# Kernel tuning notes

Hardware: AMD Instinct MI355X
Metric: run time of the kernel (lower is better)

## Reference

```python
import jax, jax.numpy as jnp
import numpy as np

# Fixed graph/model dims (see shape_source)
C = 16      # cardinality
SUB = 64    # representation_size // cardinality
R = 1024    # representation_size
E = 1024    # node_encoding_size
S = 1024    # processed spatial feature size
G = 256     # global (FPN) channels
NH = 64     # number of human nodes
N = 256     # total number of nodes (humans first)
P = NH * N  # number of (human, node) pairs
EPS = 1e-5


def _layernorm(x, g, b):
    mu = jnp.mean(x, axis=-1, keepdims=True)
    var = jnp.var(x, axis=-1, keepdims=True)
    return (x - mu) * jax.lax.rsqrt(var + EPS) * g + b


def _pair_head(app, spat, W1, b1, W2, b2, W3, b3):
    # app: [P_or_1, A], spat: [P, S] -> [P, R]  (sum over cardinality; NO outer relu)
    a1 = jnp.einsum('pi,cis->cps', app, W1) + b1[:, None, :]   # [C,P_or_1,SUB]
    a2 = jnp.einsum('pj,cjs->cps', spat, W2) + b2[:, None, :]  # [C,P,SUB]
    h = jax.nn.relu(a1 * a2)                                   # broadcast over P
    return jnp.einsum('cps,csr->pr', h, W3) + jnp.sum(b3, axis=0)


def reference(node_encodings, spatial_raw, global_feat,
              sp_W1, sp_b1, sp_W2, sp_b2, sp_W3, sp_b3,
              ah_W1, ah_b1, ah_W2, ah_b2, ah_W3, ah_b3,
              o2s_W1, o2s_b1, o2s_W2, o2s_b2, o2s_W3, o2s_b3,
              s2o_W1, s2o_b1, s2o_W2, s2o_b2, s2o_W3, s2o_b3,
              ahg_W1, ahg_b1, ahg_W2, ahg_b2, ahg_W3, ahg_b3,
              adj_W, adj_b, lnh_g, lnh_b, lno_g, lno_b):
    # spatial head MLP: 36 -> 128 -> 256 -> 1024 with ReLU
    sp = jax.nn.relu(spatial_raw @ sp_W1 + sp_b1)
    sp = jax.nn.relu(sp @ sp_W2 + sp_b2)
    sp = jax.nn.relu(sp @ sp_W3 + sp_b3)            # [P, S]
    sp3 = sp.reshape(NH, N, S)                      # [NH, N, S]

    x_idx = jnp.repeat(jnp.arange(NH), N)           # [P]
    y_idx = jnp.tile(jnp.arange(N), NH)             # [P]

    h_enc = node_encodings[:NH]                     # humans are permuted to the top
    o_enc = node_encodings

    for _ in range(1):  # num_iter
        app_pairs = jnp.concatenate([h_enc[x_idx], o_enc[y_idx]], axis=1)  # [P, 2E]
        weights = jax.nn.relu(_pair_head(app_pairs, sp, ah_W1, ah_b1, ah_W2, ah_b2, ah_W3, ah_b3))
        adj = (weights @ adj_W + adj_b).reshape(NH, N)

        # obj_to_sub (node_type='object'): appearance = all node encodings
        a1 = jnp.einsum('ni,cis->cns', o_enc, o2s_W1) + o2s_b1[:, None, :]          # [C,N,SUB]
        a2 = jnp.einsum('hnj,cjs->chns', sp3, o2s_W2) + o2s_b2[:, None, None, :]    # [C,NH,N,SUB]
        m = jnp.einsum('chns,csr->hnr', jax.nn.relu(a1[:, None] * a2), o2s_W3) + jnp.sum(o2s_b3, axis=0)
        msg_h = jax.nn.relu(jnp.sum(jax.nn.softmax(adj, axis=1)[..., None] * m, axis=1))  # [NH,R]
        h_enc = _layernorm(h_enc + msg_h, lnh_g, lnh_b)

        # sub_to_obj (node_type='human'): appearance = human encodings
        a1 = jnp.einsum('hi,cis->chs', h_enc, s2o_W1) + s2o_b1[:, None, :]          # [C,NH,SUB]
        a2 = jnp.einsum('hnj,cjs->cnhs', sp3, s2o_W2) + s2o_b2[:, None, None, :]    # [C,N,NH,SUB]
        m = jnp.einsum('cnhs,csr->nhr', jax.nn.relu(a1[:, None] * a2), s2o_W3) + jnp.sum(s2o_b3, axis=0)
        msg_o = jax.nn.relu(jnp.sum(jax.nn.softmax(adj.T, axis=1)[..., None] * m, axis=1))  # [N,R]
        o_enc = _layernorm(o_enc + msg_o, lno_g, lno_b)

    app_final = jnp.concatenate([h_enc[x_idx], o_enc[y_idx]], axis=1)               # [P, 2E]
    f_local = jax.nn.relu(_pair_head(app_final, sp, ah_W1, ah_b1, ah_W2, ah_b2, ah_W3, ah_b3))
    f_glob = jax.nn.relu(_pair_head(global_feat, sp, ahg_W1, ahg_b1, ahg_W2, ahg_b2, ahg_W3, ahg_b3))
    return jnp.concatenate([f_local, f_glob], axis=1)  # [P, 2R]


def setup_inputs() -> dict:
    key = jax.random.key(0)
    ks = iter(jax.random.split(key, 64))
    def rn(shape, scale=0.05):
        return jax.random.normal(next(ks), shape, dtype=jnp.float32) * scale
    inp = {
        'node_encodings': jax.random.normal(next(ks), (N, E), dtype=jnp.float32),
        'spatial_raw': jax.random.normal(next(ks), (P, 36), dtype=jnp.float32),
        'global_feat': jax.random.normal(next(ks), (1, G), dtype=jnp.float32),
        'sp_W1': rn((36, 128)), 'sp_b1': jnp.zeros(128, jnp.float32),
        'sp_W2': rn((128, 256)), 'sp_b2': jnp.zeros(256, jnp.float32),
        'sp_W3': rn((256, S)), 'sp_b3': jnp.zeros(S, jnp.float32),
        'ah_W1': rn((C, 2 * E, SUB)), 'ah_b1': jnp.zeros((C, SUB), jnp.float32),
        'ah_W2': rn((C, S, SUB)), 'ah_b2': jnp.zeros((C, SUB), jnp.float32),
        'ah_W3': rn((C, SUB, R)), 'ah_b3': jnp.zeros((C, R), jnp.float32),
        'o2s_W1': rn((C, E, SUB)), 'o2s_b1': jnp.zeros((C, SUB), jnp.float32),
        'o2s_W2': rn((C, S, SUB)), 'o2s_b2': jnp.zeros((C, SUB), jnp.float32),
        'o2s_W3': rn((C, SUB, R)), 'o2s_b3': jnp.zeros((C, R), jnp.float32),
        's2o_W1': rn((C, E, SUB)), 's2o_b1': jnp.zeros((C, SUB), jnp.float32),
        's2o_W2': rn((C, S, SUB)), 's2o_b2': jnp.zeros((C, SUB), jnp.float32),
        's2o_W3': rn((C, SUB, R)), 's2o_b3': jnp.zeros((C, R), jnp.float32),
        'ahg_W1': rn((C, G, SUB)), 'ahg_b1': jnp.zeros((C, SUB), jnp.float32),
        'ahg_W2': rn((C, S, SUB)), 'ahg_b2': jnp.zeros((C, SUB), jnp.float32),
        'ahg_W3': rn((C, SUB, R)), 'ahg_b3': jnp.zeros((C, R), jnp.float32),
        'adj_W': rn((R, 1)), 'adj_b': jnp.zeros(1, jnp.float32),
        'lnh_g': jnp.ones(E, jnp.float32), 'lnh_b': jnp.zeros(E, jnp.float32),
        'lno_g': jnp.ones(E, jnp.float32), 'lno_b': jnp.zeros(E, jnp.float32),
    }
    return inp
```

## Files before the change

### kernel.cpp

```cpp
#include <hip/hip_runtime.h>
#include <hip/hip_bf16.h>
#include <stdint.h>
#include <stddef.h>

using bf16 = __hip_bfloat16;
typedef __bf16 bf16x8 __attribute__((ext_vector_type(8)));
typedef float f32x4 __attribute__((ext_vector_type(4)));

#define P_  16384

__device__ __forceinline__ void gload16(const void* g, void* l) {
    __builtin_amdgcn_global_load_lds((const __attribute__((address_space(1))) void*)g,
                                     (__attribute__((address_space(3))) void*)l, 16, 0, 0);
}

template<int MODE, bool RELU, bool BIAS>
__global__ __launch_bounds__(256, 3)
void gemm_bt(const bf16* __restrict__ A, const bf16* __restrict__ B,
             void* __restrict__ C, const float* __restrict__ bias,
             const float* __restrict__ aux1, const float* __restrict__ aux2,
             int M, int N, int K, int ldc, int kchunk)
{
    __shared__ __align__(16) bf16 As[128 * 32];
    __shared__ __align__(16) bf16 Bs[128 * 32];

    const int tid  = threadIdx.x;
    const int wave = tid >> 6;
    const int lane = tid & 63;
    const int tileM = blockIdx.x * 128;
    const int tileN = blockIdx.y * 128;
    const int wr = (wave >> 1) << 6;
    const int wc = (wave & 1) << 6;

    f32x4 acc[4][4] = {};

    int arow[2], brow[2], ako[2];
    #pragma unroll
    for (int j = 0; j < 2; ++j) {
        int c  = wave * 128 + j * 64 + lane;
        int r  = c >> 2;
        ako[j] = (c & 3) << 3;
        int gr = tileM + r; if (gr > M - 1) gr = M - 1;
        arow[j] = gr;
        int gn = tileN + r; if (gn > N - 1) gn = N - 1;
        brow[j] = gn;
    }
    const int m0   = wr + (lane & 15);
    const int n0   = wc + (lane & 15);
    const int koff = (lane >> 4) << 3;

    int kbeg = 0, kend = K;
    if constexpr (MODE == 2) { kbeg = blockIdx.z * kchunk; kend = kbeg + kchunk; }

    for (int k0 = kbeg; k0 < kend; k0 += 32) {
        #pragma unroll
        for (int j = 0; j < 2; ++j) {
            int c = wave * 128 + j * 64 + lane;
            gload16(A + (size_t)arow[j] * K + k0 + ako[j], (void*)(As + c * 8));
            gload16(B + (size_t)brow[j] * K + k0 + ako[j], (void*)(Bs + c * 8));
        }
        __syncthreads();
        bf16x8 af[4], bfv[4];
        #pragma unroll
        for (int i = 0; i < 4; ++i) {
            af[i]  = *(const bf16x8*)(As + (m0 + i * 16) * 32 + koff);
            bfv[i] = *(const bf16x8*)(Bs + (n0 + i * 16) * 32 + koff);
        }
        #pragma unroll
        for (int i = 0; i < 4; ++i)
            #pragma unroll
            for (int j = 0; j < 4; ++j)
                acc[i][j] = __builtin_amdgcn_mfma_f32_16x16x32_bf16(af[i], bfv[j], acc[i][j], 0, 0, 0);
        __syncthreads();
    }

    const int rbase = tileM + wr + ((lane >> 4) << 2);
    const int cbase = tileN + wc + (lane & 15);

    if constexpr (MODE == 0 || MODE == 1) {
        #pragma unroll
        for (int i = 0; i < 4; ++i)
            #pragma unroll
            for (int j = 0; j < 4; ++j)
                #pragma unroll
                for (int r = 0; r < 4; ++r) {
                    int grow = rbase + i * 16 + r;
                    if (grow >= M) continue;
                    int gcol = cbase + j * 16;
                    float v = acc[i][j][r];
                    if (BIAS) v += bias[gcol];
                    if (RELU) v = fmaxf(v, 0.f);
                    if (MODE == 1) ((bf16*)C)[(size_t)grow * ldc + gcol] = __float2bfloat16(v);
                    else           ((float*)C)[(size_t)grow * ldc + gcol] = v;
                }
    } else if constexpr (MODE == 2) {
        #pragma unroll
        for (int i = 0; i < 4; ++i)
            #pragma unroll
            for (int j = 0; j < 4; ++j)
                #pragma unroll
                for (int r = 0; r < 4; ++r) {
                    int grow = rbase + i * 16 + r;
                    if (grow >= M) continue;
                    atomicAdd((float*)C + (size_t)grow * ldc + cbase + j * 16, acc[i][j][r]);
                }
    } else if constexpr (MODE >= 3 && MODE <= 5) {
        #pragma unroll
        for (int i = 0; i < 4; ++i)
            #pragma unroll
            for (int j = 0; j < 4; ++j)
                #pragma unroll
                for (int r = 0; r < 4; ++r) {
                    int p    = rbase + i * 16 + r;
                    int gcol = cbase + j * 16;
                    float a2v = acc[i][j][r] + bias[gcol];
                    float a1v;
                    if (MODE == 3) a1v = aux1[((size_t)(p & 255) << 10) + gcol] + aux2[gcol];
                    if (MODE == 4) a1v = aux1[((size_t)(p >> 8)  << 10) + gcol] + aux2[gcol];
                    if (MODE == 5) a1v = aux1[gcol];
                    float h = fmaxf(a1v * a2v, 0.f);
                    size_t orow = (MODE == 4) ? (size_t)((p & 255) * 64 + (p >> 8)) : (size_t)p;
                    ((bf16*)C)[orow * 1024 + gcol] = __float2bfloat16(h);
                }
    } else if constexpr (MODE == 6) {
        #pragma unroll
        for (int i = 0; i < 4; ++i)
            #pragma unroll
            for (int r = 0; r < 4; ++r) {
                float s = 0.f;
                #pragma unroll
                for (int j = 0; j < 4; ++j) {
                    int gcol = cbase + j * 16;
                    s += fmaxf(acc[i][j][r] + bias[gcol], 0.f) * aux1[gcol];
                }
                s += __shfl_xor(s, 1); s += __shfl_xor(s, 2);
                s += __shfl_xor(s, 4); s += __shfl_xor(s, 8);
                if ((lane & 15) == 0)
                    atomicAdd((float*)C + rbase + i * 16 + r, s);
            }
    } else {
        float s[4] = {0.f, 0.f, 0.f, 0.f};
        #pragma unroll
        for (int i = 0; i < 4; ++i)
            #pragma unroll
            for (int r = 0; r < 4; ++r) {
                float wv = aux1[rbase + i * 16 + r];
                #pragma unroll
                for (int j = 0; j < 4; ++j) s[j] += wv * acc[i][j][r];
            }
        #pragma unroll
        for (int j = 0; j < 4; ++j) {
            s[j] += __shfl_xor(s[j], 16);
            s[j] += __shfl_xor(s[j], 32);
        }
        if (lane < 16) {
            int outrow = (tileM + wr) >> (MODE == 7 ? 8 : 6);
            #pragma unroll
            for (int j = 0; j < 4; ++j)
                atomicAdd((float*)C + (size_t)outrow * 1024 + cbase + j * 16, s[j]);
        }
    }
}

__global__ void transp(const float* __restrict__ src, bf16* __restrict__ dst,
                       int rows, int cols, size_t sstride, size_t dstride)
{
    const float* s = src + blockIdx.z * sstride;
    bf16*        d = dst + blockIdx.z * dstride;
    __shared__ float tile[32][33];
    int c0 = blockIdx.x * 32, r0 = blockIdx.y * 32;
    int x = threadIdx.x, y = threadIdx.y;
    for (int yy = y; yy < 32; yy += 8) {
        int r = r0 + yy, c = c0 + x;
        tile[yy][x] = (r < rows && c < cols) ? s[(size_t)r * cols + c] : 0.f;
    }
    __syncthreads();
    for (int yy = y; yy < 32; yy += 8) {
        int c = c0 + yy, r = r0 + x;
        if (c < cols && r < rows) d[(size_t)c * rows + r] = __float2bfloat16(tile[x][yy]);
    }
}

__global__ void conv_spw1(const float* __restrict__ src, bf16* __restrict__ dst) {
    int i = blockIdx.x * 256 + threadIdx.x;
    if (i >= 128 * 64) return;
    int k = i & 63, n = i >> 6;
    dst[i] = __float2bfloat16(k < 36 ? src[k * 128 + n] : 0.f);
}

__global__ void pad_spatial(const float* __restrict__ src, bf16* __restrict__ dst) {
    int i = blockIdx.x * 256 + threadIdx.x;
    int k = i & 63, p = i >> 6;
    dst[i] = __float2bfloat16(k < 36 ? src[p * 36 + k] : 0.f);
}

__global__ void cast_f2b(const float* __restrict__ src, bf16* __restrict__ dst, int n) {
    int i = blockIdx.x * 256 + threadIdx.x;
    if (i < n) dst[i] = __float2bfloat16(src[i]);
}

__global__ void sumb3_k(const float* __restrict__ b3, float* __restrict__ out) {
    int r = blockIdx.x * 256 + threadIdx.x;
    float s = 0.f;
    #pragma unroll
    for (int c = 0; c < 16; ++c) s += b3[c * 1024 + r];
    out[r] = s;
}

__global__ void hbuild(const float* __restrict__ Ah, const float* __restrict__ Ao,
                       const float* __restrict__ b1, const bf16* __restrict__ a2,
                       bf16* __restrict__ H)
{
    size_t base = ((size_t)blockIdx.x * 256 + threadIdx.x) * 8;
    int cs = (int)(base & 1023);
    int p  = (int)(base >> 10);
    const float* ph = Ah + ((size_t)(p >> 8) << 10) + cs;
    const float* po = Ao + ((size_t)(p & 255) << 10) + cs;
    bf16x8 av = *(const bf16x8*)(a2 + base);
    bf16x8 o;
    #pragma unroll
    for (int j = 0; j < 8; ++j) {
        float a1 = ph[j] + po[j] + b1[cs + j];
        o[j] = (__bf16)fmaxf(a1 * (float)av[j], 0.f);
    }
    *(bf16x8*)(H + base) = o;
}

__global__ void softmax_h(const float* __restrict__ adj, float* __restrict__ sh) {
    int h = blockIdx.x, n = threadIdx.x;
    __shared__ float red[256];
    float v = adj[h * 256 + n];
    red[n] = v; __syncthreads();
    for (int s = 128; s > 0; s >>= 1) { if (n < s) red[n] = fmaxf(red[n], red[n + s]); __syncthreads(); }
    float m = red[0]; __syncthreads();
    float e = expf(v - m);
    red[n] = e; __syncthreads();
    for (int s = 128; s > 0; s >>= 1) { if (n < s) red[n] += red[n + s]; __syncthreads(); }
    sh[h * 256 + n] = e / red[0];
}

__global__ void softmax_o(const float* __restrict__ adj, float* __restrict__ so) {
    int n = blockIdx.x, h = threadIdx.x;
    float v = adj[h * 256 + n];
    float m = v;
    #pragma unroll
    for (int off = 32; off; off >>= 1) m = fmaxf(m, __shfl_xor(m, off));
    float e = expf(v - m);
    float s = e;
    #pragma unroll
    for (int off = 32; off; off >>= 1) s += __shfl_xor(s, off);
    so[n * 64 + h] = e / s;
}

__global__ void ln_k(const float* __restrict__ x, const float* __restrict__ msgraw,
                     const float* __restrict__ sb3,
                     const float* __restrict__ g, const float* __restrict__ bb,
                     bf16* __restrict__ out)
{
    int row = blockIdx.x, t = threadIdx.x;
    const float* xr = x + (size_t)row * 1024;
    const float* mr = msgraw + (size_t)row * 1024;
    float v[4]; float s = 0.f, ss = 0.f;
    #pragma unroll
    for (int j = 0; j < 4; ++j) {
        int i = t + j * 256;
        v[j] = xr[i] + fmaxf(mr[i] + sb3[i], 0.f);
        s += v[j]; ss += v[j] * v[j];
    }
    __shared__ float r1[256], r2[256];
    r1[t] = s; r2[t] = ss; __syncthreads();
    for (int k = 128; k > 0; k >>= 1) { if (t < k) { r1[t] += r1[t + k]; r2[t] += r2[t + k]; } __syncthreads(); }
    float mean = r1[0] * (1.f / 1024.f);
    float var  = r2[0] * (1.f / 1024.f) - mean * mean;
    float inv  = rsqrtf(var + 1e-5f);
    #pragma unroll
    for (int j = 0; j < 4; ++j) {
        int i = t + j * 256;
        out[(size_t)row * 1024 + i] = __float2bfloat16((v[j] - mean) * inv * g[i] + bb[i]);
    }
}

__global__ void a1g_k(const float* __restrict__ gf, const float* __restrict__ W1,
                      const float* __restrict__ b1, float* __restrict__ a1g)
{
    int cs = blockIdx.x * 256 + threadIdx.x;
    int c = cs >> 6, s = cs & 63;
    float acc = b1[cs];
    for (int g = 0; g < 256; ++g) acc += gf[g] * W1[((size_t)c * 256 + g) * 64 + s];
    a1g[cs] = acc;
}

extern "C" void kernel_launch(void* const* d_in, const int* in_sizes, int n_in,
                              void* d_out, int out_size, void* d_ws, size_t ws_size,
                              hipStream_t stream)
{
    const float* node_enc = (const float*)d_in[0];
    const float* spatial  = (const float*)d_in[1];
    const float* gfeat    = (const float*)d_in[2];
    const float* sp_W1 = (const float*)d_in[3];  const float* sp_b1 = (const float*)d_in[4];
    const float* sp_W2 = (const float*)d_in[5];  const float* sp_b2 = (const float*)d_in[6];
    const float* sp_W3 = (const float*)d_in[7];  const float* sp_b3 = (const float*)d_in[8];
    const float* ah_W1 = (const float*)d_in[9];  const float* ah_b1 = (const float*)d_in[10];
    const float* ah_W2 = (const float*)d_in[11]; const float* ah_b2 = (const float*)d_in[12];
    const float* ah_W3 = (const float*)d_in[13]; const float* ah_b3 = (const float*)d_in[14];
    const float* o2s_W1 = (const float*)d_in[15]; const float* o2s_b1 = (const float*)d_in[16];
    const float* o2s_W2 = (const float*)d_in[17]; const float* o2s_b2 = (const float*)d_in[18];
    const float* o2s_W3 = (const float*)d_in[19]; const float* o2s_b3 = (const float*)d_in[20];
    const float* s2o_W1 = (const float*)d_in[21]; const float* s2o_b1 = (const float*)d_in[22];
    const float* s2o_W2 = (const float*)d_in[23]; const float* s2o_b2 = (const float*)d_in[24];
    const float* s2o_W3 = (const float*)d_in[25]; const float* s2o_b3 = (const float*)d_in[26];
    const float* ahg_W1 = (const float*)d_in[27]; const float* ahg_b1 = (const float*)d_in[28];
    const float* ahg_W2 = (const float*)d_in[29]; const float* ahg_b2 = (const float*)d_in[30];
    const float* ahg_W3 = (const float*)d_in[31]; const float* ahg_b3 = (const float*)d_in[32];
    const float* adj_W = (const float*)d_in[33];
    const float* lnh_g = (const float*)d_in[35]; const float* lnh_b = (const float*)d_in[36];
    const float* lno_g = (const float*)d_in[37]; const float* lno_b = (const float*)d_in[38];

    char* w = (char*)d_ws;
    auto alloc = [&](size_t bytes) { char* p = w; w += (bytes + 255) & ~(size_t)255; return p; };
    bf16*  sp      = (bf16*)alloc((size_t)P_ * 1024 * 2);
    bf16*  a2_ah   = (bf16*)alloc((size_t)P_ * 1024 * 2);
    bf16*  Hbuf    = (bf16*)alloc((size_t)P_ * 1024 * 2);
    bf16*  spat_pad= (bf16*)alloc((size_t)P_ * 64 * 2);
    bf16*  spL1    = (bf16*)alloc((size_t)P_ * 128 * 2);
    bf16*  spL2    = (bf16*)alloc((size_t)P_ * 256 * 2);
    bf16*  enc_bf  = (bf16*)alloc(256 * 1024 * 2);
    bf16*  henc_bf = (bf16*)alloc(64 * 1024 * 2);
    bf16*  oenc_bf = (bf16*)alloc(256 * 1024 * 2);
    bf16*  spW1t   = (bf16*)alloc(128 * 64 * 2);
    bf16*  spW2t   = (bf16*)alloc(256 * 128 * 2);
    bf16*  spW3t   = (bf16*)alloc(1024 * 256 * 2);
    bf16*  ahW1tT  = (bf16*)alloc(1024 * 1024 * 2);
    bf16*  ahW1tB  = (bf16*)alloc(1024 * 1024 * 2);
    bf16*  ahW2t   = (bf16*)alloc(1024 * 1024 * 2);
    bf16*  ahW3t   = (bf16*)alloc(1024 * 1024 * 2);
    bf16*  o2sW1t  = (bf16*)alloc(1024 * 1024 * 2);
    bf16*  o2sW2t  = (bf16*)alloc(1024 * 1024 * 2);
    bf16*  o2sW3t  = (bf16*)alloc(1024 * 1024 * 2);
    bf16*  s2oW1t  = (bf16*)alloc(1024 * 1024 * 2);
    bf16*  s2oW2t  = (bf16*)alloc(1024 * 1024 * 2);
    bf16*  s2oW3t  = (bf16*)alloc(1024 * 1024 * 2);
    bf16*  ahgW2t  = (bf16*)alloc(1024 * 1024 * 2);
    bf16*  ahgW3t  = (bf16*)alloc(1024 * 1024 * 2);
    float* Ah    = (float*)alloc(64 * 1024 * 4);
    float* Ao    = (float*)alloc(256 * 1024 * 4);
    float* a1o2s = (float*)alloc(256 * 1024 * 4);
    float* a1s2o = (float*)alloc(64 * 1024 * 4);
    float* a1g   = (float*)alloc(1024 * 4);
    float* adjv  = (float*)alloc(P_ * 4);
    float* sh    = (float*)alloc(P_ * 4);
    float* so    = (float*)alloc(P_ * 4);
    float* msgh  = (float*)alloc(64 * 1024 * 4);
    float* msgo  = (float*)alloc(256 * 1024 * 4);
    float* sb3_ah  = (float*)alloc(4096);
    float* sb3_o2s = (float*)alloc(4096);
    float* sb3_s2o = (float*)alloc(4096);
    float* sb3_ahg = (float*)alloc(4096);

    hipMemsetAsync(Ah,   0, (64 + 256 + 256 + 64) * 1024 * 4, stream);
    hipMemsetAsync(adjv, 0, P_ * 4, stream);
    hipMemsetAsync(msgh, 0, 64 * 1024 * 4, stream);
    hipMemsetAsync(msgo, 0, 256 * 1024 * 4, stream);

    dim3 tb(32, 8);
    conv_spw1<<<32, 256, 0, stream>>>(sp_W1, spW1t);
    transp<<<dim3(8, 4, 1),  tb, 0, stream>>>(sp_W2, spW2t, 128, 256, 0, 0);
    transp<<<dim3(32, 8, 1), tb, 0, stream>>>(sp_W3, spW3t, 256, 1024, 0, 0);
    transp<<<dim3(2, 32, 16), tb, 0, stream>>>(ah_W1,                     ahW1tT, 1024, 64, (size_t)2048 * 64, (size_t)64 * 1024);
    transp<<<dim3(2, 32, 16), tb, 0, stream>>>(ah_W1 + (size_t)1024 * 64, ahW1tB, 1024, 64, (size_t)2048 * 64, (size_t)64 * 1024);
    transp<<<dim3(2, 32, 16), tb, 0, stream>>>(ah_W2,  ahW2t,  1024, 64, 65536, 65536);
    transp<<<dim3(2, 32, 16), tb, 0, stream>>>(o2s_W1, o2sW1t, 1024, 64, 65536, 65536);
    transp<<<dim3(2, 32, 16), tb, 0, stream>>>(o2s_W2, o2sW2t, 1024, 64, 65536, 65536);
    transp<<<dim3(2, 32, 16), tb, 0, stream>>>(s2o_W1, s2oW1t, 1024, 64, 65536, 65536);
    transp<<<dim3(2, 32, 16), tb, 0, stream>>>(s2o_W2, s2oW2t, 1024, 64, 65536, 65536);
    transp<<<dim3(2, 32, 16), tb, 0, stream>>>(ahg_W2, ahgW2t, 1024, 64, 65536, 65536);
    transp<<<dim3(32, 32, 1), tb, 0, stream>>>(ah_W3,  ahW3t,  1024, 1024, 0, 0);
    transp<<<dim3(32, 32, 1), tb, 0, stream>>>(o2s_W3, o2sW3t, 1024, 1024, 0, 0);
    transp<<<dim3(32, 32, 1), tb, 0, stream>>>(s2o_W3, s2oW3t, 1024, 1024, 0, 0);
    transp<<<dim3(32, 32, 1), tb, 0, stream>>>(ahg_W3, ahgW3t, 1024, 1024, 0, 0);
    pad_spatial<<<4096, 256, 0, stream>>>(spatial, spat_pad);
    cast_f2b<<<1024, 256, 0, stream>>>(node_enc, enc_bf, 256 * 1024);
    sumb3_k<<<4, 256, 0, stream>>>(ah_b3,  sb3_ah);
    sumb3_k<<<4, 256, 0, stream>>>(o2s_b3, sb3_o2s);
    sumb3_k<<<4, 256, 0, stream>>>(s2o_b3, sb3_s2o);
    sumb3_k<<<4, 256, 0, stream>>>(ahg_b3, sb3_ahg);
    a1g_k<<<4, 256, 0, stream>>>(gfeat, ahg_W1, ahg_b1, a1g);

    #define G128(M, N) dim3(((M) + 127) / 128, (N) / 128), dim3(256)
    #define GSPL(M)    dim3(((M) + 127) / 128, 8, 8), dim3(256)

    gemm_bt<1, true, true><<<G128(P_, 128),  0, stream>>>(spat_pad, spW1t, spL1, sp_b1, nullptr, nullptr, P_, 128, 64, 128, 0);
    gemm_bt<1, true, true><<<G128(P_, 256),  0, stream>>>(spL1,     spW2t, spL2, sp_b2, nullptr, nullptr, P_, 256, 128, 256, 0);
    gemm_bt<1, true, true><<<G128(P_, 1024), 0, stream>>>(spL2,     spW3t, sp,   sp_b3, nullptr, nullptr, P_, 1024, 256, 1024, 0);

    gemm_bt<1, false, true><<<G128(P_, 1024), 0, stream>>>(sp, ahW2t, a2_ah, ah_b2, nullptr, nullptr, P_, 1024, 1024, 1024, 0);

    gemm_bt<2, false, false><<<GSPL(64),  0, stream>>>(enc_bf, ahW1tT, Ah, nullptr, nullptr, nullptr, 64,  1024, 1024, 1024, 128);
    gemm_bt<2, false, false><<<GSPL(256), 0, stream>>>(enc_bf, ahW1tB, Ao, nullptr, nullptr, nullptr, 256, 1024, 1024, 1024, 128);
    hbuild<<<8192, 256, 0, stream>>>(Ah, Ao, ah_b1, a2_ah, Hbuf);
    gemm_bt<6, false, false><<<G128(P_, 1024), 0, stream>>>(Hbuf, ahW3t, adjv, sb3_ah, adj_W, nullptr, P_, 1024, 1024, 1024, 0);
    softmax_h<<<64, 256, 0, stream>>>(adjv, sh);
    softmax_o<<<256, 64, 0, stream>>>(adjv, so);

    gemm_bt<2, false, false><<<GSPL(256), 0, stream>>>(enc_bf, o2sW1t, a1o2s, nullptr, nullptr, nullptr, 256, 1024, 1024, 1024, 128);
    gemm_bt<3, false, false><<<G128(P_, 1024), 0, stream>>>(sp, o2sW2t, Hbuf, o2s_b2, a1o2s, o2s_b1, P_, 1024, 1024, 1024, 0);
    gemm_bt<7, false, false><<<G128(P_, 1024), 0, stream>>>(Hbuf, o2sW3t, msgh, nullptr, sh, nullptr, P_, 1024, 1024, 1024, 0);
    ln_k<<<64, 256, 0, stream>>>(node_enc, msgh, sb3_o2s, lnh_g, lnh_b, henc_bf);

    gemm_bt<2, false, false><<<GSPL(64), 0, stream>>>(henc_bf, s2oW1t, a1s2o, nullptr, nullptr, nullptr, 64, 1024, 1024, 1024, 128);
    gemm_bt<4, false, false><<<G128(P_, 1024), 0, stream>>>(sp, s2oW2t, Hbuf, s2o_b2, a1s2o, s2o_b1, P_, 1024, 1024, 1024, 0);
    gemm_bt<8, false, false><<<G128(P_, 1024), 0, stream>>>(Hbuf, s2oW3t, msgo, nullptr, so, nullptr, P_, 1024, 1024, 1024, 0);
    ln_k<<<256, 256, 0, stream>>>(node_enc, msgo, sb3_s2o, lno_g, lno_b, oenc_bf);

    hipMemsetAsync(Ah, 0, (64 + 256) * 1024 * 4, stream);
    gemm_bt<2, false, false><<<GSPL(64),  0, stream>>>(henc_bf, ahW1tT, Ah, nullptr, nullptr, nullptr, 64,  1024, 1024, 1024, 128);
    gemm_bt<2, false, false><<<GSPL(256), 0, stream>>>(oenc_bf, ahW1tB, Ao, nullptr, nullptr, nullptr, 256, 1024, 1024, 1024, 128);
    hbuild<<<8192, 256, 0, stream>>>(Ah, Ao, ah_b1, a2_ah, Hbuf);
    gemm_bt<0, true, true><<<G128(P_, 1024), 0, stream>>>(Hbuf, ahW3t, (float*)d_out, sb3_ah, nullptr, nullptr, P_, 1024, 1024, 2048, 0);

    gemm_bt<5, false, false><<<G128(P_, 1024), 0, stream>>>(sp, ahgW2t, Hbuf, ahg_b2, a1g, nullptr, P_, 1024, 1024, 1024, 0);
    gemm_bt<0, true, true><<<G128(P_, 1024), 0, stream>>>(Hbuf, ahgW3t, (float*)d_out + 1024, sb3_ahg, nullptr, nullptr, P_, 1024, 1024, 2048, 0);

    (void)in_sizes; (void)n_in; (void)out_size; (void)ws_size;
}
```

Measured before the change: 849.0 us.

## Batch W2 projections into one wide GEMM and merge W1 GEMMs and transposes

Concatenates the ah, o2s and ahg W2 weights so the spatial features are read once by a single N=3072 GEMM. Its epilogue writes a2_ah, the o2s hidden tensor and the ahg hidden tensor in one pass. W1 projections that share an input are merged into wider split-K GEMMs with smaller K chunks, and many small transpose, bias-sum and memset launches are batched into single kernels. This cuts repeated reads of the large sp activation and per-launch overhead. In exchange it allocates two extra P×1024 bf16 buffers and adds a branchy epilogue.

```diff
diff --git a/kernel.cpp b/kernel.cpp
--- a/kernel.cpp
+++ b/kernel.cpp
@@ -14,12 +14,20 @@
                                      (__attribute__((address_space(3))) void*)l, 16, 0, 0);
 }
 
+struct GArgs {
+    const bf16* A; const bf16* B; void* C;
+    const float* bias;
+    const float* aux1;
+    const float* aux2;
+    int M, N, K, ldc, kchunk, aux_ld;
+    void* C2; void* C3;
+    const float* b2a; const float* b2b; const float* b2c;
+    const float* b1o;  const float* a1gv;
+};
+
 template<int MODE, bool RELU, bool BIAS>
 __global__ __launch_bounds__(256, 3)
-void gemm_bt(const bf16* __restrict__ A, const bf16* __restrict__ B,
-             void* __restrict__ C, const float* __restrict__ bias,
-             const float* __restrict__ aux1, const float* __restrict__ aux2,
-             int M, int N, int K, int ldc, int kchunk)
+void gemm_bt(GArgs g)
 {
     __shared__ __align__(16) bf16 As[128 * 32];
     __shared__ __align__(16) bf16 Bs[128 * 32];
@@ -31,6 +39,7 @@
     const int tileN = blockIdx.y * 128;
     const int wr = (wave >> 1) << 6;
     const int wc = (wave & 1) << 6;
+    const int M = g.M, N = g.N, K = g.K;
 
     f32x4 acc[4][4] = {};
 
@@ -50,14 +59,14 @@
     const int koff = (lane >> 4) << 3;
 
     int kbeg = 0, kend = K;
-    if constexpr (MODE == 2) { kbeg = blockIdx.z * kchunk; kend = kbeg + kchunk; }
+    if constexpr (MODE == 2) { kbeg = blockIdx.z * g.kchunk; kend = kbeg + g.kchunk; }
 
     for (int k0 = kbeg; k0 < kend; k0 += 32) {
         #pragma unroll
         for (int j = 0; j < 2; ++j) {
             int c = wave * 128 + j * 64 + lane;
-            gload16(A + (size_t)arow[j] * K + k0 + ako[j], (void*)(As + c * 8));
-            gload16(B + (size_t)brow[j] * K + k0 + ako[j], (void*)(Bs + c * 8));
+            gload16(g.A + (size_t)arow[j] * K + k0 + ako[j], (void*)(As + c * 8));
+            gload16(g.B + (size_t)brow[j] * K + k0 + ako[j], (void*)(Bs + c * 8));
         }
         __syncthreads();
         bf16x8 af[4], bfv[4];
@@ -88,10 +97,10 @@
                     if (grow >= M) continue;
                     int gcol = cbase + j * 16;
                     float v = acc[i][j][r];
-                    if (BIAS) v += bias[gcol];
+                    if (BIAS) v += g.bias[gcol];
                     if (RELU) v = fmaxf(v, 0.f);
-                    if (MODE == 1) ((bf16*)C)[(size_t)grow * ldc + gcol] = __float2bfloat16(v);
-                    else           ((float*)C)[(size_t)grow * ldc + gcol] = v;
+                    if (MODE == 1) ((bf16*)g.C)[(size_t)grow * g.ldc + gcol] = __float2bfloat16(v);
+                    else           ((float*)g.C)[(size_t)grow * g.ldc + gcol] = v;
                 }
     } else if constexpr (MODE == 2) {
         #pragma unroll
@@ -102,9 +111,9 @@
                 for (int r = 0; r < 4; ++r) {
                     int grow = rbase + i * 16 + r;
                     if (grow >= M) continue;
-                    atomicAdd((float*)C + (size_t)grow * ldc + cbase + j * 16, acc[i][j][r]);
+                    atomicAdd((float*)g.C + (size_t)grow * g.ldc + cbase + j * 16, acc[i][j][r]);
                 }
-    } else if constexpr (MODE >= 3 && MODE <= 5) {
+    } else if constexpr (MODE == 4) {
         #pragma unroll
         for (int i = 0; i < 4; ++i)
             #pragma unroll
@@ -113,14 +122,11 @@
                 for (int r = 0; r < 4; ++r) {
                     int p    = rbase + i * 16 + r;
                     int gcol = cbase + j * 16;
-                    float a2v = acc[i][j][r] + bias[gcol];
-                    float a1v;
-                    if (MODE == 3) a1v = aux1[((size_t)(p & 255) << 10) + gcol] + aux2[gcol];
-                    if (MODE == 4) a1v = aux1[((size_t)(p >> 8)  << 10) + gcol] + aux2[gcol];
-                    if (MODE == 5) a1v = aux1[gcol];
+                    float a2v = acc[i][j][r] + g.bias[gcol];
+                    float a1v = g.aux1[(size_t)(p >> 8) * g.aux_ld + gcol] + g.aux2[gcol];
                     float h = fmaxf(a1v * a2v, 0.f);
-                    size_t orow = (MODE == 4) ? (size_t)((p & 255) * 64 + (p >> 8)) : (size_t)p;
-                    ((bf16*)C)[orow * 1024 + gcol] = __float2bfloat16(h);
+                    size_t orow = (size_t)((p & 255) * 64 + (p >> 8));
+                    ((bf16*)g.C)[orow * 1024 + gcol] = __float2bfloat16(h);
                 }
     } else if constexpr (MODE == 6) {
         #pragma unroll
@@ -131,20 +137,20 @@
                 #pragma unroll
                 for (int j = 0; j < 4; ++j) {
                     int gcol = cbase + j * 16;
-                    s += fmaxf(acc[i][j][r] + bias[gcol], 0.f) * aux1[gcol];
+                    s += fmaxf(acc[i][j][r] + g.bias[gcol], 0.f) * g.aux1[gcol];
                 }
                 s += __shfl_xor(s, 1); s += __shfl_xor(s, 2);
                 s += __shfl_xor(s, 4); s += __shfl_xor(s, 8);
                 if ((lane & 15) == 0)
-                    atomicAdd((float*)C + rbase + i * 16 + r, s);
+                    atomicAdd((float*)g.C + rbase + i * 16 + r, s);
             }
-    } else {
+    } else if constexpr (MODE == 7 || MODE == 8) {
         float s[4] = {0.f, 0.f, 0.f, 0.f};
         #pragma unroll
         for (int i = 0; i < 4; ++i)
             #pragma unroll
             for (int r = 0; r < 4; ++r) {
-                float wv = aux1[rbase + i * 16 + r];
+                float wv = g.aux1[rbase + i * 16 + r];
                 #pragma unroll
                 for (int j = 0; j < 4; ++j) s[j] += wv * acc[i][j][r];
             }
@@ -157,9 +163,45 @@
             int outrow = (tileM + wr) >> (MODE == 7 ? 8 : 6);
             #pragma unroll
             for (int j = 0; j < 4; ++j)
-                atomicAdd((float*)C + (size_t)outrow * 1024 + cbase + j * 16, s[j]);
+                atomicAdd((float*)g.C + (size_t)outrow * 1024 + cbase + j * 16, s[j]);
         }
-    }
+    } else if constexpr (MODE == 9) {
+        int grp = tileN >> 10;
+        int lcb = (tileN & 1023) + wc + (lane & 15);
+        #pragma unroll
+        for (int i = 0; i < 4; ++i)
+            #pragma unroll
+            for (int j = 0; j < 4; ++j)
+                #pragma unroll
+                for (int r = 0; r < 4; ++r) {
+                    int p    = rbase + i * 16 + r;
+                    int lcol = lcb + j * 16;
+                    float accv = acc[i][j][r];
+                    if (grp == 0) {
+                        ((bf16*)g.C)[(size_t)p * 1024 + lcol] =
+                            __float2bfloat16(accv + g.b2a[lcol]);
+                    } else if (grp == 1) {
+                        float a2v = accv + g.b2b[lcol];
+                        float a1v = g.aux1[(size_t)(p & 255) * g.aux_ld + lcol] + g.b1o[lcol];
+                        ((bf16*)g.C2)[(size_t)p * 1024 + lcol] =
+                            __float2bfloat16(fmaxf(a1v * a2v, 0.f));
+                    } else {
+                        float a2v = accv + g.b2c[lcol];
+                        ((bf16*)g.C3)[(size_t)p * 1024 + lcol] =
+                            __float2bfloat16(fmaxf(g.a1gv[lcol] * a2v, 0.f));
+                    }
+                }
+    }
+}
+
+static GArgs mkargs(const bf16* A, const bf16* B, void* C, const float* bias,
+                    const float* aux1, const float* aux2,
+                    int M, int N, int K, int ldc, int kchunk, int aux_ld)
+{
+    GArgs g{};
+    g.A = A; g.B = B; g.C = C; g.bias = bias; g.aux1 = aux1; g.aux2 = aux2;
+    g.M = M; g.N = N; g.K = K; g.ldc = ldc; g.kchunk = kchunk; g.aux_ld = aux_ld;
+    return g;
 }
 
 __global__ void transp(const float* __restrict__ src, bf16* __restrict__ dst,
@@ -181,6 +223,37 @@
     }
 }
 
+struct T8 { const float* s[8]; bf16* d[8]; size_t ss[8]; };
+__global__ void transp64b(T8 t)
+{
+    int pair = blockIdx.z >> 4, slice = blockIdx.z & 15;
+    const float* s = t.s[pair] + slice * t.ss[pair];
+    bf16*        d = t.d[pair] + slice * 65536;
+    __shared__ float tile[32][33];
+    int c0 = blockIdx.x * 32, r0 = blockIdx.y * 32;
+    int x = threadIdx.x, y = threadIdx.y;
+    for (int yy = y; yy < 32; yy += 8)
+        tile[yy][x] = s[(size_t)(r0 + yy) * 64 + c0 + x];
+    __syncthreads();
+    for (int yy = y; yy < 32; yy += 8)
+        d[(size_t)(c0 + yy) * 1024 + r0 + x] = __float2bfloat16(tile[x][yy]);
+}
+
+struct T4 { const float* s[4]; bf16* d[4]; };
+__global__ void transp1024b(T4 t)
+{
+    const float* s = t.s[blockIdx.z];
+    bf16*        d = t.d[blockIdx.z];
+    __shared__ float tile[32][33];
+    int c0 = blockIdx.x * 32, r0 = blockIdx.y * 32;
+    int x = threadIdx.x, y = threadIdx.y;
+    for (int yy = y; yy < 32; yy += 8)
+        tile[yy][x] = s[(size_t)(r0 + yy) * 1024 + c0 + x];
+    __syncthreads();
+    for (int yy = y; yy < 32; yy += 8)
+        d[(size_t)(c0 + yy) * 1024 + r0 + x] = __float2bfloat16(tile[x][yy]);
+}
+
 __global__ void conv_spw1(const float* __restrict__ src, bf16* __restrict__ dst) {
     int i = blockIdx.x * 256 + threadIdx.x;
     if (i >= 128 * 64) return;
@@ -199,23 +272,27 @@
     if (i < n) dst[i] = __float2bfloat16(src[i]);
 }
 
-__global__ void sumb3_k(const float* __restrict__ b3, float* __restrict__ out) {
-    int r = blockIdx.x * 256 + threadIdx.x;
+struct S4 { const float* s[4]; float* d[4]; };
+__global__ void sumb3b(S4 a) {
+    int i = blockIdx.x * 256 + threadIdx.x;
+    int pair = i >> 10, r = i & 1023;
+    const float* b3 = a.s[pair];
     float s = 0.f;
     #pragma unroll
     for (int c = 0; c < 16; ++c) s += b3[c * 1024 + r];
-    out[r] = s;
-}
-
-__global__ void hbuild(const float* __restrict__ Ah, const float* __restrict__ Ao,
+    a.d[pair][r] = s;
+}
+
+__global__ void hbuild(const float* __restrict__ Ah, int ah_ld,
+                       const float* __restrict__ Ao, int ao_ld,
                        const float* __restrict__ b1, const bf16* __restrict__ a2,
                        bf16* __restrict__ H)
 {
     size_t base = ((size_t)blockIdx.x * 256 + threadIdx.x) * 8;
     int cs = (int)(base & 1023);
     int p  = (int)(base >> 10);
-    const float* ph = Ah + ((size_t)(p >> 8) << 10) + cs;
-    const float* po = Ao + ((size_t)(p & 255) << 10) + cs;
+    const float* ph = Ah + (size_t)(p >> 8) * ah_ld + cs;
+    const float* po = Ao + (size_t)(p & 255) * ao_ld + cs;
     bf16x8 av = *(const bf16x8*)(a2 + base);
     bf16x8 o;
     #pragma unroll
@@ -321,6 +398,8 @@
     bf16*  sp      = (bf16*)alloc((size_t)P_ * 1024 * 2);
     bf16*  a2_ah   = (bf16*)alloc((size_t)P_ * 1024 * 2);
     bf16*  Hbuf    = (bf16*)alloc((size_t)P_ * 1024 * 2);
+    bf16*  H_o2s   = (bf16*)alloc((size_t)P_ * 1024 * 2);
+    bf16*  H_ahg   = (bf16*)alloc((size_t)P_ * 1024 * 2);
     bf16*  spat_pad= (bf16*)alloc((size_t)P_ * 64 * 2);
     bf16*  spL1    = (bf16*)alloc((size_t)P_ * 128 * 2);
     bf16*  spL2    = (bf16*)alloc((size_t)P_ * 256 * 2);
@@ -330,96 +409,116 @@
     bf16*  spW1t   = (bf16*)alloc(128 * 64 * 2);
     bf16*  spW2t   = (bf16*)alloc(256 * 128 * 2);
     bf16*  spW3t   = (bf16*)alloc(1024 * 256 * 2);
-    bf16*  ahW1tT  = (bf16*)alloc(1024 * 1024 * 2);
-    bf16*  ahW1tB  = (bf16*)alloc(1024 * 1024 * 2);
-    bf16*  ahW2t   = (bf16*)alloc(1024 * 1024 * 2);
+    bf16*  W2cat   = (bf16*)alloc((size_t)3072 * 1024 * 2);
+    bf16*  W1catB  = (bf16*)alloc((size_t)2048 * 1024 * 2);
+    bf16*  W1catF  = (bf16*)alloc((size_t)2048 * 1024 * 2);
+    bf16*  s2oW2t  = (bf16*)alloc(1024 * 1024 * 2);
     bf16*  ahW3t   = (bf16*)alloc(1024 * 1024 * 2);
-    bf16*  o2sW1t  = (bf16*)alloc(1024 * 1024 * 2);
-    bf16*  o2sW2t  = (bf16*)alloc(1024 * 1024 * 2);
     bf16*  o2sW3t  = (bf16*)alloc(1024 * 1024 * 2);
-    bf16*  s2oW1t  = (bf16*)alloc(1024 * 1024 * 2);
-    bf16*  s2oW2t  = (bf16*)alloc(1024 * 1024 * 2);
     bf16*  s2oW3t  = (bf16*)alloc(1024 * 1024 * 2);
-    bf16*  ahgW2t  = (bf16*)alloc(1024 * 1024 * 2);
     bf16*  ahgW3t  = (bf16*)alloc(1024 * 1024 * 2);
     float* Ah    = (float*)alloc(64 * 1024 * 4);
-    float* Ao    = (float*)alloc(256 * 1024 * 4);
-    float* a1o2s = (float*)alloc(256 * 1024 * 4);
-    float* a1s2o = (float*)alloc(64 * 1024 * 4);
-    float* a1g   = (float*)alloc(1024 * 4);
+    float* Aoa1  = (float*)alloc(256 * 2048 * 4);
+    float* A1f   = (float*)alloc(64 * 2048 * 4);
+    float* Ao_f  = (float*)alloc(256 * 1024 * 4);
+    size_t z1_bytes = (size_t)(64 * 1024 + 256 * 2048 + 64 * 2048 + 256 * 1024) * 4 + 1024;
     float* adjv  = (float*)alloc(P_ * 4);
+    float* msgh  = (float*)alloc(64 * 1024 * 4);
+    float* msgo  = (float*)alloc(256 * 1024 * 4);
+    size_t z2_bytes = (size_t)(P_ + 64 * 1024 + 256 * 1024) * 4 + 1024;
     float* sh    = (float*)alloc(P_ * 4);
     float* so    = (float*)alloc(P_ * 4);
-    float* msgh  = (float*)alloc(64 * 1024 * 4);
-    float* msgo  = (float*)alloc(256 * 1024 * 4);
+    float* a1g   = (float*)alloc(1024 * 4);
     float* sb3_ah  = (float*)alloc(4096);
     float* sb3_o2s = (float*)alloc(4096);
     float* sb3_s2o = (float*)alloc(4096);
     float* sb3_ahg = (float*)alloc(4096);
 
-    hipMemsetAsync(Ah,   0, (64 + 256 + 256 + 64) * 1024 * 4, stream);
-    hipMemsetAsync(adjv, 0, P_ * 4, stream);
-    hipMemsetAsync(msgh, 0, 64 * 1024 * 4, stream);
-    hipMemsetAsync(msgo, 0, 256 * 1024 * 4, stream);
-
+    hipMemsetAsync(Ah,   0, z1_bytes, stream);
+    hipMemsetAsync(adjv, 0, z2_bytes, stream);
+
+    {
+        T8 t;
+        t.s[0] = ah_W1;                     t.d[0] = W1catF + (size_t)1024 * 1024; t.ss[0] = (size_t)2048 * 64;
+        t.s[1] = ah_W1 + (size_t)1024 * 64; t.d[1] = W1catB;                       t.ss[1] = (size_t)2048 * 64;
+        t.s[2] = o2s_W1;                    t.d[2] = W1catB + (size_t)1024 * 1024; t.ss[2] = 65536;
+        t.s[3] = s2o_W1;                    t.d[3] = W1catF;                       t.ss[3] = 65536;
+        t.s[4] = ah_W2;                     t.d[4] = W2cat;                        t.ss[4] = 65536;
+        t.s[5] = o2s_W2;                    t.d[5] = W2cat + (size_t)1024 * 1024;  t.ss[5] = 65536;
+        t.s[6] = ahg_W2;                    t.d[6] = W2cat + (size_t)2048 * 1024;  t.ss[6] = 65536;
+        t.s[7] = s2o_W2;                    t.d[7] = s2oW2t;                       t.ss[7] = 65536;
+        transp64b<<<dim3(2, 32, 128), dim3(32, 8), 0, stream>>>(t);
+    }
+    {
+        T4 t;
+        t.s[0] = ah_W3;  t.d[0] = ahW3t;
+        t.s[1] = o2s_W3; t.d[1] = o2sW3t;
+        t.s[2] = s2o_W3; t.d[2] = s2oW3t;
+        t.s[3] = ahg_W3; t.d[3] = ahgW3t;
+        transp1024b<<<dim3(32, 32, 4), dim3(32, 8), 0, stream>>>(t);
+    }
     dim3 tb(32, 8);
     conv_spw1<<<32, 256, 0, stream>>>(sp_W1, spW1t);
     transp<<<dim3(8, 4, 1),  tb, 0, stream>>>(sp_W2, spW2t, 128, 256, 0, 0);
     transp<<<dim3(32, 8, 1), tb, 0, stream>>>(sp_W3, spW3t, 256, 1024, 0, 0);
-    transp<<<dim3(2, 32, 16), tb, 0, stream>>>(ah_W1,                     ahW1tT, 1024, 64, (size_t)2048 * 64, (size_t)64 * 1024);
-    transp<<<dim3(2, 32, 16), tb, 0, stream>>>(ah_W1 + (size_t)1024 * 64, ahW1tB, 1024, 64, (size_t)2048 * 64, (size_t)64 * 1024);
-    transp<<<dim3(2, 32, 16), tb, 0, stream>>>(ah_W2,  ahW2t,  1024, 64, 65536, 65536);
-    transp<<<dim3(2, 32, 16), tb, 0, stream>>>(o2s_W1, o2sW1t, 1024, 64, 65536, 65536);
-    transp<<<dim3(2, 32, 16), tb, 0, stream>>>(o2s_W2, o2sW2t, 1024, 64, 65536, 65536);
-    transp<<<dim3(2, 32, 16), tb, 0, stream>>>(s2o_W1, s2oW1t, 1024, 64, 65536, 65536);
-    transp<<<dim3(2, 32, 16), tb, 0, stream>>>(s2o_W2, s2oW2t, 1024, 64, 65536, 65536);
-    transp<<<dim3(2, 32, 16), tb, 0, stream>>>(ahg_W2, ahgW2t, 1024, 64, 65536, 65536);
-    transp<<<dim3(32, 32, 1), tb, 0, stream>>>(ah_W3,  ahW3t,  1024, 1024, 0, 0);
-    transp<<<dim3(32, 32, 1), tb, 0, stream>>>(o2s_W3, o2sW3t, 1024, 1024, 0, 0);
-    transp<<<dim3(32, 32, 1), tb, 0, stream>>>(s2o_W3, s2oW3t, 1024, 1024, 0, 0);
-    transp<<<dim3(32, 32, 1), tb, 0, stream>>>(ahg_W3, ahgW3t, 1024, 1024, 0, 0);
     pad_spatial<<<4096, 256, 0, stream>>>(spatial, spat_pad);
     cast_f2b<<<1024, 256, 0, stream>>>(node_enc, enc_bf, 256 * 1024);
-    sumb3_k<<<4, 256, 0, stream>>>(ah_b3,  sb3_ah);
-    sumb3_k<<<4, 256, 0, stream>>>(o2s_b3, sb3_o2s);
-    sumb3_k<<<4, 256, 0, stream>>>(s2o_b3, sb3_s2o);
-    sumb3_k<<<4, 256, 0, stream>>>(ahg_b3, sb3_ahg);
+    {
+        S4 a;
+        a.s[0] = ah_b3;  a.d[0] = sb3_ah;
+        a.s[1] = o2s_b3; a.d[1] = sb3_o2s;
+        a.s[2] = s2o_b3; a.d[2] = sb3_s2o;
+        a.s[3] = ahg_b3; a.d[3] = sb3_ahg;
+        sumb3b<<<16, 256, 0, stream>>>(a);
+    }
     a1g_k<<<4, 256, 0, stream>>>(gfeat, ahg_W1, ahg_b1, a1g);
 
-    #define G128(M, N) dim3(((M) + 127) / 128, (N) / 128), dim3(256)
-    #define GSPL(M)    dim3(((M) + 127) / 128, 8, 8), dim3(256)
-
-    gemm_bt<1, true, true><<<G128(P_, 128),  0, stream>>>(spat_pad, spW1t, spL1, sp_b1, nullptr, nullptr, P_, 128, 64, 128, 0);
-    gemm_bt<1, true, true><<<G128(P_, 256),  0, stream>>>(spL1,     spW2t, spL2, sp_b2, nullptr, nullptr, P_, 256, 128, 256, 0);
-    gemm_bt<1, true, true><<<G128(P_, 1024), 0, stream>>>(spL2,     spW3t, sp,   sp_b3, nullptr, nullptr, P_, 1024, 256, 1024, 0);
-
-    gemm_bt<1, false, true><<<G128(P_, 1024), 0, stream>>>(sp, ahW2t, a2_ah, ah_b2, nullptr, nullptr, P_, 1024, 1024, 1024, 0);
-
-    gemm_bt<2, false, false><<<GSPL(64),  0, stream>>>(enc_bf, ahW1tT, Ah, nullptr, nullptr, nullptr, 64,  1024, 1024, 1024, 128);
-    gemm_bt<2, false, false><<<GSPL(256), 0, stream>>>(enc_bf, ahW1tB, Ao, nullptr, nullptr, nullptr, 256, 1024, 1024, 1024, 128);
-    hbuild<<<8192, 256, 0, stream>>>(Ah, Ao, ah_b1, a2_ah, Hbuf);
-    gemm_bt<6, false, false><<<G128(P_, 1024), 0, stream>>>(Hbuf, ahW3t, adjv, sb3_ah, adj_W, nullptr, P_, 1024, 1024, 1024, 0);
+    gemm_bt<2, false, false><<<dim3(2, 16, 16), 256, 0, stream>>>(
+        mkargs(enc_bf, W1catB, Aoa1, nullptr, nullptr, nullptr, 256, 2048, 1024, 2048, 64, 0));
+    gemm_bt<2, false, false><<<dim3(1, 8, 16), 256, 0, stream>>>(
+        mkargs(enc_bf, W1catF + (size_t)1024 * 1024, Ah, nullptr, nullptr, nullptr, 64, 1024, 1024, 1024, 64, 0));
+
+    gemm_bt<1, true, true><<<dim3(128, 1), 256, 0, stream>>>(
+        mkargs(spat_pad, spW1t, spL1, sp_b1, nullptr, nullptr, P_, 128, 64, 128, 0, 0));
+    gemm_bt<1, true, true><<<dim3(128, 2), 256, 0, stream>>>(
+        mkargs(spL1, spW2t, spL2, sp_b2, nullptr, nullptr, P_, 256, 128, 256, 0, 0));
+    gemm_bt<1, true, true><<<dim3(128, 8), 256, 0, stream>>>(
+        mkargs(spL2, spW3t, sp, sp_b3, nullptr, nullptr, P_, 1024, 256, 1024, 0, 0));
+
+    {
+        GArgs g = mkargs(sp, W2cat, a2_ah, nullptr, Aoa1 + 1024, nullptr, P_, 3072, 1024, 1024, 0, 2048);
+        g.C2 = H_o2s; g.C3 = H_ahg;
+        g.b2a = ah_b2; g.b2b = o2s_b2; g.b2c = ahg_b2; g.b1o = o2s_b1; g.a1gv = a1g;
+        gemm_bt<9, false, false><<<dim3(128, 24), 256, 0, stream>>>(g);
+    }
+
+    hbuild<<<8192, 256, 0, stream>>>(Ah, 1024, Aoa1, 2048, ah_b1, a2_ah, Hbuf);
+    gemm_bt<6, false, false><<<dim3(128, 8), 256, 0, stream>>>(
+        mkargs(Hbuf, ahW3t, adjv, sb3_ah, adj_W, nullptr, P_, 1024, 1024, 1024, 0, 0));
     softmax_h<<<64, 256, 0, stream>>>(adjv, sh);
     softmax_o<<<256, 64, 0, stream>>>(adjv, so);
 
-    gemm_bt<2, false, false><<<GSPL(256), 0, stream>>>(enc_bf, o2sW1t, a1o2s, nullptr, nullptr, nullptr, 256, 1024, 1024, 1024, 128);
-    gemm_bt<3, false, false><<<G128(P_, 1024), 0, stream>>>(sp, o2sW2t, Hbuf, o2s_b2, a1o2s, o2s_b1, P_, 1024, 1024, 1024, 0);
-    gemm_bt<7, false, false><<<G128(P_, 1024), 0, stream>>>(Hbuf, o2sW3t, msgh, nullptr, sh, nullptr, P_, 1024, 1024, 1024, 0);
+    gemm_bt<7, false, false><<<dim3(128, 8), 256, 0, stream>>>(
+        mkargs(H_o2s, o2sW3t, msgh, nullptr, sh, nullptr, P_, 1024, 1024, 1024, 0, 0));
     ln_k<<<64, 256, 0, stream>>>(node_enc, msgh, sb3_o2s, lnh_g, lnh_b, henc_bf);
 
-    gemm_bt<2, false, false><<<GSPL(64), 0, stream>>>(henc_bf, s2oW1t, a1s2o, nullptr, nullptr, nullptr, 64, 1024, 1024, 1024, 128);
-    gemm_bt<4, false, false><<<G128(P_, 1024), 0, stream>>>(sp, s2oW2t, Hbuf, s2o_b2, a1s2o, s2o_b1, P_, 1024, 1024, 1024, 0);
-    gemm_bt<8, false, false><<<G128(P_, 1024), 0, stream>>>(Hbuf, s2oW3t, msgo, nullptr, so, nullptr, P_, 1024, 1024, 1024, 0);
+    gemm_bt<2, false, false><<<dim3(1, 16, 16), 256, 0, stream>>>(
+        mkargs(henc_bf, W1catF, A1f, nullptr, nullptr, nullptr, 64, 2048, 1024, 2048, 64, 0));
+
+    gemm_bt<4, false, false><<<dim3(128, 8), 256, 0, stream>>>(
+        mkargs(sp, s2oW2t, H_o2s , s2o_b2, A1f, s2o_b1, P_, 1024, 1024, 1024, 0, 2048));
+    gemm_bt<8, false, false><<<dim3(128, 8), 256, 0, stream>>>(
+        mkargs(H_o2s, s2oW3t, msgo, nullptr, so, nullptr, P_, 1024, 1024, 1024, 0, 0));
     ln_k<<<256, 256, 0, stream>>>(node_enc, msgo, sb3_s2o, lno_g, lno_b, oenc_bf);
 
-    hipMemsetAsync(Ah, 0, (64 + 256) * 1024 * 4, stream);
-    gemm_bt<2, false, false><<<GSPL(64),  0, stream>>>(henc_bf, ahW1tT, Ah, nullptr, nullptr, nullptr, 64,  1024, 1024, 1024, 128);
-    gemm_bt<2, false, false><<<GSPL(256), 0, stream>>>(oenc_bf, ahW1tB, Ao, nullptr, nullptr, nullptr, 256, 1024, 1024, 1024, 128);
-    hbuild<<<8192, 256, 0, stream>>>(Ah, Ao, ah_b1, a2_ah, Hbuf);
-    gemm_bt<0, true, true><<<G128(P_, 1024), 0, stream>>>(Hbuf, ahW3t, (float*)d_out, sb3_ah, nullptr, nullptr, P_, 1024, 1024, 2048, 0);
-
-    gemm_bt<5, false, false><<<G128(P_, 1024), 0, stream>>>(sp, ahgW2t, Hbuf, ahg_b2, a1g, nullptr, P_, 1024, 1024, 1024, 0);
-    gemm_bt<0, true, true><<<G128(P_, 1024), 0, stream>>>(Hbuf, ahgW3t, (float*)d_out + 1024, sb3_ahg, nullptr, nullptr, P_, 1024, 1024, 2048, 0);
+    gemm_bt<2, false, false><<<dim3(2, 8, 16), 256, 0, stream>>>(
+        mkargs(oenc_bf, W1catB, Ao_f, nullptr, nullptr, nullptr, 256, 1024, 1024, 1024, 64, 0));
+    hbuild<<<8192, 256, 0, stream>>>(A1f + 1024, 2048, Ao_f, 1024, ah_b1, a2_ah, Hbuf);
+    gemm_bt<0, true, true><<<dim3(128, 8), 256, 0, stream>>>(
+        mkargs(Hbuf, ahW3t, (float*)d_out, sb3_ah, nullptr, nullptr, P_, 1024, 1024, 2048, 0, 0));
+
+    gemm_bt<0, true, true><<<dim3(128, 8), 256, 0, stream>>>(
+        mkargs(H_ahg, ahgW3t, (float*)d_out + 1024, sb3_ahg, nullptr, nullptr, P_, 1024, 1024, 2048, 0, 0));
 
     (void)in_sizes; (void)n_in; (void)out_size; (void)ws_size;
 }
```

Result: faster. 809.8 us (-4.6%).
